# Optimization experiments

Measured on AMD Instinct MI355X. Metric: run time of the kernel, lower is better.

The kernel has to match this reference:

```python
import jax, jax.numpy as jnp
import numpy as np

# grid derived from output_shape=[1,10,200,176,128]: sparse_shape = (10+1, 200, 176)
D, H, W = 11, 200, 176
C_IN = 128
C_MID = 64
NUM_VOX = 16000
BN_EPS = 1e-5
DN = ('NCDHW', 'OIDHW', 'NCDHW')


def conv3d(x, w, stride, padding):
    return jax.lax.conv_general_dilated(x, w, window_strides=stride,
                                        padding=padding, dimension_numbers=DN)


def setup_inputs() -> dict:
    key = jax.random.key(0)
    ks = jax.random.split(key, 12)
    voxel_features = jax.random.normal(ks[0], (NUM_VOX, C_IN), dtype=jnp.float32)
    # unique active voxel coords (batch, z, y, x)
    lin = jax.random.choice(ks[1], D * H * W, (NUM_VOX,), replace=False)
    z = lin // (H * W)
    r = lin % (H * W)
    y = r // W
    x = r % W
    b = jnp.zeros((NUM_VOX,), dtype=jnp.int32)
    coors = jnp.stack([b, z.astype(jnp.int32), y.astype(jnp.int32), x.astype(jnp.int32)], axis=1)
    s = 0.05
    w1 = jax.random.normal(ks[2], (C_MID, C_IN, 3, 3, 3), jnp.float32) * s   # subm0
    w2 = jax.random.normal(ks[3], (C_MID, C_MID, 3, 1, 1), jnp.float32) * s  # strided
    w3 = jax.random.normal(ks[4], (C_MID, C_MID, 3, 3, 3), jnp.float32) * s  # subm1
    w4 = jax.random.normal(ks[5], (C_MID, C_MID, 3, 3, 3), jnp.float32) * s  # subm1
    w5 = jax.random.normal(ks[6], (C_MID, C_MID, 3, 1, 1), jnp.float32) * s  # strided
    bn_gamma = 1.0 + 0.1 * jax.random.normal(ks[7], (5, C_MID), jnp.float32)
    bn_beta = 0.1 * jax.random.normal(ks[8], (5, C_MID), jnp.float32)
    bn_mean = 0.1 * jax.random.normal(ks[9], (5, C_MID), jnp.float32)
    bn_var = 1.0 + 0.1 * jax.random.uniform(ks[10], (5, C_MID), jnp.float32)
    return {"voxel_features": voxel_features, "w1": w1, "w2": w2, "w3": w3,
            "w4": w4, "w5": w5, "bn_gamma": bn_gamma, "bn_beta": bn_beta,
            "bn_mean": bn_mean, "bn_var": bn_var, "coors": coors, "batch_size": 1}


def _bn_relu(x, i, mask, bn_gamma, bn_beta, bn_mean, bn_var):
    # inference-mode BatchNorm1d over active voxels (mask keeps inactive sites at 0)
    scale = (bn_gamma[i] / jnp.sqrt(bn_var[i] + BN_EPS))[None, :, None, None, None]
    shift = (bn_beta[i] - bn_mean[i] * bn_gamma[i] / jnp.sqrt(bn_var[i] + BN_EPS))[None, :, None, None, None]
    return jnp.maximum(x * scale + shift, 0.0) * mask


def reference(voxel_features, w1, w2, w3, w4, w5, bn_gamma, bn_beta, bn_mean, bn_var, coors, batch_size):
    N = int(batch_size)
    b, z, y, x = coors[:, 0], coors[:, 1], coors[:, 2], coors[:, 3]
    dense = jnp.zeros((N, C_IN, D, H, W), voxel_features.dtype).at[b, :, z, y, x].set(voxel_features)
    mask = jnp.zeros((N, 1, D, H, W), voxel_features.dtype).at[b, :, z, y, x].set(1.0)
    ones_k = jnp.ones((1, 1, 3, 1, 1), voxel_features.dtype)

    # SubMConv3d(128->64, k3, pad1): dense conv then restrict to active input sites
    h = conv3d(dense, w1, (1, 1, 1), [(1, 1), (1, 1), (1, 1)]) * mask
    h = _bn_relu(h, 0, mask, bn_gamma, bn_beta, bn_mean, bn_var)

    # SparseConv3d(64->64, k=(3,1,1), s=(2,1,1), pad0): new active set
    h = conv3d(h, w2, (2, 1, 1), 'VALID')
    mask = (conv3d(mask, ones_k, (2, 1, 1), 'VALID') > 0).astype(h.dtype)
    h = _bn_relu(h, 1, mask, bn_gamma, bn_beta, bn_mean, bn_var)

    # SubMConv3d(64->64) x2
    h = conv3d(h, w3, (1, 1, 1), [(1, 1), (1, 1), (1, 1)]) * mask
    h = _bn_relu(h, 2, mask, bn_gamma, bn_beta, bn_mean, bn_var)
    h = conv3d(h, w4, (1, 1, 1), [(1, 1), (1, 1), (1, 1)]) * mask
    h = _bn_relu(h, 3, mask, bn_gamma, bn_beta, bn_mean, bn_var)

    # SparseConv3d(64->64, (3,1,1), (2,1,1))
    h = conv3d(h, w5, (2, 1, 1), 'VALID')
    mask = (conv3d(mask, ones_k, (2, 1, 1), 'VALID') > 0).astype(h.dtype)
    h = _bn_relu(h, 4, mask, bn_gamma, bn_beta, bn_mean, bn_var)

    n, c, d, hh, ww = h.shape  # (1, 64, 2, 200, 176)
    return h.reshape(n, c * d, hh, ww)
```

## Files before the change

kernel.cpp:

```cpp
#include <hip/hip_runtime.h>

constexpr int D0  = 11;
constexpr int Hh  = 200;
constexpr int Ww  = 176;
constexpr int HWC = Hh * Ww;
constexpr int NV  = 16000;
constexpr int ND1 = 5;
constexpr int ND2 = 2;
constexpr int CAPN = 32000;
constexpr float EPS = 1e-5f;

constexpr int CAP1P  = 432000;
constexpr int CAP34P = 864000;
constexpr int CAP2P  = 32000;
constexpr int CAP5P  = 64000;

#define PC(i) ((i) << 5)

__device__ inline void wave_count(bool has, int* counter) {
    unsigned long long m = __ballot(has);
    int lane = threadIdx.x & 63;
    if (m && lane == __builtin_ctzll(m)) atomicAdd(counter, (int)__popcll(m));
}

__device__ inline int wave_append(bool has, int* counter) {
    unsigned long long m = __ballot(has);
    if (!m) return -1;
    int lane = threadIdx.x & 63;
    int leader = __builtin_ctzll(m);
    int base = 0;
    if (lane == leader) base = atomicAdd(counter, (int)__popcll(m));
    base = __shfl(base, leader);
    return has ? base + (int)__popcll(m & ((1ull << lane) - 1)) : -1;
}

__device__ inline int block_append(bool has, int* counter, int* lds) {
    int tid = threadIdx.x;
    int w = tid >> 6, lane = tid & 63;
    unsigned long long m = __ballot(has);
    if (lane == 0) lds[w] = (int)__popcll(m);
    __syncthreads();
    if (tid == 0) {
        int t0 = lds[0], t1 = lds[1], t2 = lds[2], t3 = lds[3];
        int base = atomicAdd(counter, t0 + t1 + t2 + t3);
        lds[4] = base;
        lds[5] = base + t0;
        lds[6] = base + t0 + t1;
        lds[7] = base + t0 + t1 + t2;
    }
    __syncthreads();
    int base = lds[4 + w];
    return has ? base + (int)__popcll(m & ((1ull << lane) - 1)) : -1;
}

__global__ __launch_bounds__(256) void setup1_k(const int* __restrict__ coors,
    int* __restrict__ grid0,
    const float* __restrict__ w1, const float* __restrict__ w2,
    const float* __restrict__ w3, const float* __restrict__ w4,
    const float* __restrict__ w5,
    float* __restrict__ w1t, float* __restrict__ w2t, float* __restrict__ w3t,
    float* __restrict__ w4t, float* __restrict__ w5t) {
    int idx = blockIdx.x * 256 + threadIdx.x;
    int role = blockIdx.y;
    if (role == 0) {
        if (idx < NV) {
            int4 c = reinterpret_cast<const int4*>(coors)[idx];
            grid0[c.y * HWC + c.z * Ww + c.w] = idx;
        }
        return;
    }
    const float* src; float* dst; int I, K;
    switch (role) {
        case 1:  src = w1; dst = w1t; I = 128; K = 27; break;
        case 2:  src = w2; dst = w2t; I = 64;  K = 3;  break;
        case 3:  src = w3; dst = w3t; I = 64;  K = 27; break;
        case 4:  src = w4; dst = w4t; I = 64;  K = 27; break;
        default: src = w5; dst = w5t; I = 64;  K = 3;  break;
    }
    int tot = 64 * I * K;
    if (idx >= tot) return;
    int o = idx / (I * K), r = idx % (I * K), ii = r / K, k = r % K;
    dst[(k * I + ii) * 64 + o] = src[idx];
}

__global__ __launch_bounds__(256) void setup2_k(const int* __restrict__ coors,
    const int* __restrict__ grid0, int* __restrict__ grid1,
    int* __restrict__ list1, int* __restrict__ list2, int* __restrict__ ctr) {
    __shared__ int lds[8];
    int idx = blockIdx.x * 256 + threadIdx.x;
    int role = blockIdx.y;
    if (role == 0) {
        bool occ = false; int p = idx;
        if (p < ND1 * HWC) {
            int d1 = p / HWC, yx = p - d1 * HWC;
            int b = (2 * d1) * HWC + yx;
            occ = (grid0[b] >= 0) || (grid0[b + HWC] >= 0) || (grid0[b + 2 * HWC] >= 0);
        }
        int s = block_append(occ, ctr + PC(0), lds);
        if (occ) { grid1[p] = s; list1[s] = p; }
    } else if (role == 1) {
        bool occ = false; int p = idx;
        if (p < ND2 * HWC) {
            int d2 = p / HWC, yx = p - d2 * HWC;
            #pragma unroll
            for (int dd = 0; dd < 7; ++dd) occ |= (grid0[(4 * d2 + dd) * HWC + yx] >= 0);
        }
        int s = block_append(occ, ctr + PC(1), lds);
        if (occ) list2[s] = p;
    } else {
        int k = idx / NV;
        bool has = false;
        if (idx < 27 * NV) {
            int i = idx - k * NV;
            int4 c = reinterpret_cast<const int4*>(coors)[i];
            int kd = k / 9, r = k % 9, kh = r / 3, kw = r % 3;
            int zz = c.y + kd - 1, yy = c.z + kh - 1, xx = c.w + kw - 1;
            if ((unsigned)zz < (unsigned)D0 && (unsigned)yy < (unsigned)Hh &&
                (unsigned)xx < (unsigned)Ww)
                has = grid0[zz * HWC + yy * Ww + xx] >= 0;
        }
        wave_count(has, ctr + PC(2 + k));
    }
}

__global__ __launch_bounds__(256) void setup3_k(const int* __restrict__ grid0,
    const int* __restrict__ grid1, const int* __restrict__ list1,
    const int* __restrict__ list2, int* __restrict__ ctr) {
    int idx = blockIdx.x * 256 + threadIdx.x;
    int role = blockIdx.y;
    int n1 = ctr[PC(0)], n2 = ctr[PC(1)];
    if (role == 0) {
        int k = idx / CAPN; bool has = false;
        if (idx < 3 * CAPN) {
            int s1 = idx - k * CAPN;
            if (s1 < n1) {
                int p = list1[s1]; int d1 = p / HWC, yx = p - d1 * HWC;
                has = grid0[(2 * d1 + k) * HWC + yx] >= 0;
            }
        }
        wave_count(has, ctr + PC(29 + k));
    } else if (role == 1) {
        int k = idx / CAPN; bool has = false;
        if (idx < 27 * CAPN) {
            int s1 = idx - k * CAPN;
            if (s1 < n1) {
                int p = list1[s1];
                int d1 = p / HWC, yx = p - d1 * HWC, y = yx / Ww, x = yx - y * Ww;
                int kd = k / 9, r = k % 9, kh = r / 3, kw = r % 3;
                int dd = d1 + kd - 1, yy = y + kh - 1, xx = x + kw - 1;
                if ((unsigned)dd < (unsigned)ND1 && (unsigned)yy < (unsigned)Hh &&
                    (unsigned)xx < (unsigned)Ww)
                    has = grid1[dd * HWC + yy * Ww + xx] >= 0;
            }
        }
        wave_count(has, ctr + PC(32 + k));
    } else {
        int k = idx / CAPN; bool has = false;
        if (idx < 3 * CAPN) {
            int s2 = idx - k * CAPN;
            if (s2 < n2) {
                int p = list2[s2]; int d2 = p / HWC, yx = p - d2 * HWC;
                has = grid1[(2 * d2 + k) * HWC + yx] >= 0;
            }
        }
        wave_count(has, ctr + PC(59 + k));
    }
}

__global__ __launch_bounds__(64) void setup4_k(const int* __restrict__ ctr,
    int* __restrict__ soff1, int* __restrict__ soff2,
    int* __restrict__ soff34, int* __restrict__ soff5) {
    int role = blockIdx.y, s = threadIdx.x;
    const int* cnt; int* soff; int NT, F;
    switch (role) {
        case 0:  cnt = ctr + PC(2);  soff = soff1;  NT = 27; F = 2; break;
        case 1:  cnt = ctr + PC(29); soff = soff2;  NT = 3;  F = 1; break;
        case 2:  cnt = ctr + PC(32); soff = soff34; NT = 27; F = 1; break;
        default: cnt = ctr + PC(59); soff = soff5;  NT = 3;  F = 1; break;
    }
    int tot = F * NT;
    if (s <= tot) {
        int sum = 0;
        for (int k = 0; k < NT; ++k) {
            int below = s - F * k;
            below = below < 0 ? 0 : (below > F ? F : below);
            sum += cnt[PC(k)] * below;
        }
        soff[s] = sum;
    }
}

__global__ __launch_bounds__(256) void setup5_k(const int* __restrict__ coors,
    const int* __restrict__ grid0, const int* __restrict__ grid1,
    const int* __restrict__ list1, const int* __restrict__ list2,
    int* __restrict__ ctr,
    const int* __restrict__ soff1, const int* __restrict__ soff2,
    const int* __restrict__ soff34, const int* __restrict__ soff5,
    int2* __restrict__ pairs1, int2* __restrict__ pairs2,
    int2* __restrict__ pairs34, int2* __restrict__ pairs5) {
    int idx = blockIdx.x * 256 + threadIdx.x;
    int role = blockIdx.y;
    int n1 = ctr[PC(0)], n2 = ctr[PC(1)];
    if (role == 0) {
        int k = idx / NV; bool has = false; int j = -1, i = 0;
        if (idx < 27 * NV) {
            i = idx - k * NV;
            int4 c = reinterpret_cast<const int4*>(coors)[i];
            int kd = k / 9, r = k % 9, kh = r / 3, kw = r % 3;
            int zz = c.y + kd - 1, yy = c.z + kh - 1, xx = c.w + kw - 1;
            if ((unsigned)zz < (unsigned)D0 && (unsigned)yy < (unsigned)Hh &&
                (unsigned)xx < (unsigned)Ww) {
                j = grid0[zz * HWC + yy * Ww + xx];
                has = j >= 0;
            }
        }
        int rel = wave_append(has, ctr + PC(62 + k));
        if (has) {
            int2 pr; pr.x = j; pr.y = i;
            pairs1[soff1[2 * k] + rel]     = pr;
            pairs1[soff1[2 * k + 1] + rel] = pr;
        }
    } else if (role == 1) {
        int k = idx / CAPN; bool has = false; int j = -1, s1 = 0;
        if (idx < 3 * CAPN) {
            s1 = idx - k * CAPN;
            if (s1 < n1) {
                int p = list1[s1]; int d1 = p / HWC, yx = p - d1 * HWC;
                j = grid0[(2 * d1 + k) * HWC + yx];
                has = j >= 0;
            }
        }
        int rel = wave_append(has, ctr + PC(89 + k));
        if (has) { int2 pr; pr.x = j; pr.y = s1; pairs2[soff2[k] + rel] = pr; }
    } else if (role == 2) {
        int k = idx / CAPN; bool has = false; int j = -1, s1 = 0;
        if (idx < 27 * CAPN) {
            s1 = idx - k * CAPN;
            if (s1 < n1) {
                int p = list1[s1];
                int d1 = p / HWC, yx = p - d1 * HWC, y = yx / Ww, x = yx - y * Ww;
                int kd = k / 9, r = k % 9, kh = r / 3, kw = r % 3;
                int dd = d1 + kd - 1, yy = y + kh - 1, xx = x + kw - 1;
                if ((unsigned)dd < (unsigned)ND1 && (unsigned)yy < (unsigned)Hh &&
                    (unsigned)xx < (unsigned)Ww) {
                    j = grid1[dd * HWC + yy * Ww + xx];
                    has = j >= 0;
                }
            }
        }
        int rel = wave_append(has, ctr + PC(92 + k));
        if (has) { int2 pr; pr.x = j; pr.y = s1; pairs34[soff34[k] + rel] = pr; }
    } else {
        int k = idx / CAPN; bool has = false; int j = -1, s2 = 0;
        if (idx < 3 * CAPN) {
            s2 = idx - k * CAPN;
            if (s2 < n2) {
                int p = list2[s2]; int d2 = p / HWC, yx = p - d2 * HWC;
                j = grid1[(2 * d2 + k) * HWC + yx];
                has = j >= 0;
            }
        }
        int rel = wave_append(has, ctr + PC(119 + k));
        if (has) { int2 pr; pr.x = j; pr.y = s2; pairs5[soff5[k] + rel] = pr; }
    }
}

template<int XS, bool HALF>
__global__ __launch_bounds__(256, 4) void pconv_k(
    const float* __restrict__ fin, const float* __restrict__ wt,
    const int2* __restrict__ pairs, const int* __restrict__ soff, int nslice,
    float* __restrict__ acc) {
    const int lane = threadIdx.x & 63;
    const int wid = __builtin_amdgcn_readfirstlane(
        (int)blockIdx.x * 4 + ((int)threadIdx.x >> 6));
    const int nw = (int)gridDim.x * 4;
    const int total = soff[nslice];
    int chunk = (total + nw - 1) / nw;
    int v = wid * chunk;
    int v1 = v + chunk; if (v1 > total) v1 = total;
    if (v >= v1) return;

    int lo = 0, hi = nslice - 1;
    while (lo < hi) { int mid = (lo + hi + 1) >> 1; if (soff[mid] <= v) lo = mid; else hi = mid - 1; }
    int s = lo, send = soff[s + 1];

    float w[64];
    int xofs = 0;
    bool need = true;
    while (v < v1) {
        while (v >= send) { ++s; send = soff[s + 1]; need = true; }
        if (need) {
            const float* wp = wt + (size_t)s * 4096 + lane;
            #pragma unroll
            for (int c = 0; c < 64; ++c) w[c] = wp[(size_t)c * 64];
            if (HALF) xofs = (s & 1) * 64;
            need = false;
        }
        int e = v1 < send ? v1 : send;
        for (; v + 1 < e; v += 2) {
            int2 prA = pairs[v];
            int2 prB = pairs[v + 1];
            int ja = __builtin_amdgcn_readfirstlane(prA.x);
            int ya = __builtin_amdgcn_readfirstlane(prA.y);
            int jb = __builtin_amdgcn_readfirstlane(prB.x);
            int yb = __builtin_amdgcn_readfirstlane(prB.y);
            const float* xa = fin + (size_t)ja * XS + xofs;
            const float* xb = fin + (size_t)jb * XS + xofs;
            float a0=0.f,a1=0.f,a2=0.f,a3=0.f,b0=0.f,b1=0.f,b2=0.f,b3=0.f;
            #pragma unroll
            for (int c = 0; c < 64; c += 4) {
                a0 = fmaf(xa[c],     w[c],     a0);
                a1 = fmaf(xa[c + 1], w[c + 1], a1);
                a2 = fmaf(xa[c + 2], w[c + 2], a2);
                a3 = fmaf(xa[c + 3], w[c + 3], a3);
                b0 = fmaf(xb[c],     w[c],     b0);
                b1 = fmaf(xb[c + 1], w[c + 1], b1);
                b2 = fmaf(xb[c + 2], w[c + 2], b2);
                b3 = fmaf(xb[c + 3], w[c + 3], b3);
            }
            unsafeAtomicAdd(acc + ((size_t)ya << 6) + lane, (a0 + a1) + (a2 + a3));
            unsafeAtomicAdd(acc + ((size_t)yb << 6) + lane, (b0 + b1) + (b2 + b3));
        }
        if (v < e) {
            int2 pr = pairs[v]; ++v;
            int jp = __builtin_amdgcn_readfirstlane(pr.x);
            int yp = __builtin_amdgcn_readfirstlane(pr.y);
            const float* xp = fin + (size_t)jp * XS + xofs;
            float a0=0.f,a1=0.f,a2=0.f,a3=0.f;
            #pragma unroll
            for (int c = 0; c < 64; c += 4) {
                a0 = fmaf(xp[c],     w[c],     a0);
                a1 = fmaf(xp[c + 1], w[c + 1], a1);
                a2 = fmaf(xp[c + 2], w[c + 2], a2);
                a3 = fmaf(xp[c + 3], w[c + 3], a3);
            }
            unsafeAtomicAdd(acc + ((size_t)yp << 6) + lane, (a0 + a1) + (a2 + a3));
        }
    }
}

template<bool ZERO, bool FIXEDN>
__global__ __launch_bounds__(256) void bn_k(float* __restrict__ acc,
    float* __restrict__ f, const int* __restrict__ ctr,
    const float* __restrict__ bg, const float* __restrict__ bb,
    const float* __restrict__ bm, const float* __restrict__ bv) {
    int idx = blockIdx.x * 256 + threadIdx.x;
    int site = idx >> 6, o = idx & 63;
    int n = FIXEDN ? NV : ctr[PC(0)];
    if (site < n) {
        float sc = bg[o] / sqrtf(bv[o] + EPS);
        float sh = bb[o] - bm[o] * sc;
        f[idx] = fmaxf(fmaf(acc[idx], sc, sh), 0.f);
    }
    if (ZERO) acc[idx] = 0.f;
}

__global__ __launch_bounds__(256) void bn5_k(const float* __restrict__ acc5,
    const int* __restrict__ list2, const int* __restrict__ ctr,
    const float* __restrict__ bg, const float* __restrict__ bb,
    const float* __restrict__ bm, const float* __restrict__ bv,
    float* __restrict__ out) {
    __shared__ float tile[64 * 65];
    __shared__ int pp[64];
    int n2 = ctr[PC(1)];
    int sb = blockIdx.x * 64;
    int tid = threadIdx.x;
    if (tid < 64) pp[tid] = (sb + tid < n2) ? list2[sb + tid] : -1;
    int o = tid & 63;
    float sc = bg[o] / sqrtf(bv[o] + EPS);
    float sh = bb[o] - bm[o] * sc;
    __syncthreads();
    #pragma unroll
    for (int it = 0; it < 16; ++it) {
        int sl = it * 4 + (tid >> 6);
        int s2 = sb + sl;
        if (s2 < n2)
            tile[sl * 65 + o] = fmaxf(fmaf(acc5[(size_t)s2 * 64 + o], sc, sh), 0.f);
    }
    __syncthreads();
    #pragma unroll
    for (int it = 0; it < 16; ++it) {
        int og = it * 4 + (tid >> 6);
        int sl = tid & 63;
        int p = pp[sl];
        if (p >= 0) {
            int d2 = p / HWC, yx = p - d2 * HWC;
            out[(size_t)(og * ND2 + d2) * HWC + yx] = tile[sl * 65 + og];
        }
    }
}

extern "C" void kernel_launch(void* const* d_in, const int* in_sizes, int n_in,
                              void* d_out, int out_size, void* d_ws, size_t ws_size,
                              hipStream_t stream) {
    const float* vf = (const float*)d_in[0];
    const float* w1 = (const float*)d_in[1];
    const float* w2 = (const float*)d_in[2];
    const float* w3 = (const float*)d_in[3];
    const float* w4 = (const float*)d_in[4];
    const float* w5 = (const float*)d_in[5];
    const float* bg = (const float*)d_in[6];
    const float* bb = (const float*)d_in[7];
    const float* bm = (const float*)d_in[8];
    const float* bv = (const float*)d_in[9];
    const int* coors = (const int*)d_in[10];
    float* out = (float*)d_out;

    char* ws = (char*)d_ws;
    size_t off = 0;
    auto take = [&](size_t n) -> void* {
        void* pp = ws + off;
        off += (n + 255) & ~(size_t)255;
        return pp;
    };
    int*   ctr  = (int*)take(16384);
    float* acc1 = (float*)take((size_t)NV * 64 * 4);
    float* accX = (float*)take((size_t)CAPN * 64 * 4);
    float* acc5 = (float*)take((size_t)CAPN * 64 * 4);
    size_t zero_len = (char*)acc5 + (size_t)CAPN * 64 * 4 - (char*)ctr;
    int*   grid0 = (int*)take((size_t)D0 * HWC * 4);
    int*   grid1 = (int*)take((size_t)ND1 * HWC * 4);
    size_t ff_len = (char*)grid1 + (size_t)ND1 * HWC * 4 - (char*)grid0;
    int*   list1 = (int*)take(CAPN * 4);
    int*   list2 = (int*)take(CAPN * 4);
    int*   soff1 = (int*)take(256);
    int*   soff2 = (int*)take(256);
    int*   soff34 = (int*)take(256);
    int*   soff5 = (int*)take(256);
    float* w1t = (float*)take((size_t)27 * 128 * 64 * 4);
    float* w2t = (float*)take((size_t)3 * 64 * 64 * 4);
    float* w3t = (float*)take((size_t)27 * 64 * 64 * 4);
    float* w4t = (float*)take((size_t)27 * 64 * 64 * 4);
    float* w5t = (float*)take((size_t)3 * 64 * 64 * 4);
    float* fA  = (float*)take((size_t)NV * 64 * 4);
    float* fB  = (float*)take((size_t)CAPN * 64 * 4);
    int2*  pairs1  = (int2*)take((size_t)2 * CAP1P * 8);
    int2*  pairs2  = (int2*)take((size_t)CAP2P * 8);
    int2*  pairs34 = (int2*)take((size_t)CAP34P * 8);
    int2*  pairs5  = (int2*)take((size_t)CAP5P * 8);

    hipMemsetAsync(ctr, 0x00, zero_len, stream);
    hipMemsetAsync(grid0, 0xFF, ff_len, stream);
    hipMemsetAsync(out, 0x00, (size_t)out_size * 4, stream);

    setup1_k<<<dim3(864, 6), 256, 0, stream>>>(coors, grid0, w1, w2, w3, w4, w5,
                                               w1t, w2t, w3t, w4t, w5t);
    setup2_k<<<dim3(1688, 3), 256, 0, stream>>>(coors, grid0, grid1, list1, list2, ctr);
    setup3_k<<<dim3(3375, 3), 256, 0, stream>>>(grid0, grid1, list1, list2, ctr);
    setup4_k<<<dim3(1, 4), 64, 0, stream>>>(ctr, soff1, soff2, soff34, soff5);
    setup5_k<<<dim3(3375, 4), 256, 0, stream>>>(coors, grid0, grid1, list1, list2, ctr,
                                                soff1, soff2, soff34, soff5,
                                                pairs1, pairs2, pairs34, pairs5);

    pconv_k<128, true><<<1024, 256, 0, stream>>>(vf, w1t, pairs1, soff1, 54, acc1);
    bn_k<false, true><<<(NV * 64) / 256, 256, 0, stream>>>(acc1, fA, ctr,
        bg, bb, bm, bv);
    pconv_k<64, false><<<1024, 256, 0, stream>>>(fA, w2t, pairs2, soff2, 3, accX);
    bn_k<true, false><<<(CAPN * 64) / 256, 256, 0, stream>>>(accX, fB, ctr,
        bg + 64, bb + 64, bm + 64, bv + 64);
    pconv_k<64, false><<<1024, 256, 0, stream>>>(fB, w3t, pairs34, soff34, 27, accX);
    bn_k<true, false><<<(CAPN * 64) / 256, 256, 0, stream>>>(accX, fB, ctr,
        bg + 128, bb + 128, bm + 128, bv + 128);
    pconv_k<64, false><<<1024, 256, 0, stream>>>(fB, w4t, pairs34, soff34, 27, accX);
    bn_k<false, false><<<(CAPN * 64) / 256, 256, 0, stream>>>(accX, fB, ctr,
        bg + 192, bb + 192, bm + 192, bv + 192);
    pconv_k<64, false><<<1024, 256, 0, stream>>>(fB, w5t, pairs5, soff5, 3, acc5);
    bn5_k<<<CAPN / 64, 256, 0, stream>>>(acc5, list2, ctr,
        bg + 256, bb + 256, bm + 256, bv + 256, out);
}
```

Measured before the change: 279.9 us.

## Build rulebook pairs in one pass with fixed-stride slices instead of count+scan+fill

After: 248.9 us. -11.1%, faster.

```diff
diff --git a/kernel.cpp b/kernel.cpp
--- a/kernel.cpp
+++ b/kernel.cpp
@@ -10,18 +10,7 @@
 constexpr int CAPN = 32000;
 constexpr float EPS = 1e-5f;
 
-constexpr int CAP1P  = 432000;
-constexpr int CAP34P = 864000;
-constexpr int CAP2P  = 32000;
-constexpr int CAP5P  = 64000;
-
 #define PC(i) ((i) << 5)
-
-__device__ inline void wave_count(bool has, int* counter) {
-    unsigned long long m = __ballot(has);
-    int lane = threadIdx.x & 63;
-    if (m && lane == __builtin_ctzll(m)) atomicAdd(counter, (int)__popcll(m));
-}
 
 __device__ inline int wave_append(bool has, int* counter) {
     unsigned long long m = __ballot(has);
@@ -85,12 +74,13 @@
 
 __global__ __launch_bounds__(256) void setup2_k(const int* __restrict__ coors,
     const int* __restrict__ grid0, int* __restrict__ grid1,
-    int* __restrict__ list1, int* __restrict__ list2, int* __restrict__ ctr) {
+    int* __restrict__ list1, int* __restrict__ list2, int* __restrict__ ctr,
+    int2* __restrict__ pairs1) {
     __shared__ int lds[8];
-    int idx = blockIdx.x * 256 + threadIdx.x;
-    int role = blockIdx.y;
-    if (role == 0) {
-        bool occ = false; int p = idx;
+    int bid = blockIdx.x, tid = threadIdx.x;
+    if (bid < 688) {
+        int p = bid * 256 + tid;
+        bool occ = false;
         if (p < ND1 * HWC) {
             int d1 = p / HWC, yx = p - d1 * HWC;
             int b = (2 * d1) * HWC + yx;
@@ -98,8 +88,9 @@
         }
         int s = block_append(occ, ctr + PC(0), lds);
         if (occ) { grid1[p] = s; list1[s] = p; }
-    } else if (role == 1) {
-        bool occ = false; int p = idx;
+    } else if (bid < 963) {
+        int p = (bid - 688) * 256 + tid;
+        bool occ = false;
         if (p < ND2 * HWC) {
             int d2 = p / HWC, yx = p - d2 * HWC;
             #pragma unroll
@@ -108,103 +99,11 @@
         int s = block_append(occ, ctr + PC(1), lds);
         if (occ) list2[s] = p;
     } else {
+        int idx = (bid - 963) * 256 + tid;
         int k = idx / NV;
-        bool has = false;
+        bool has = false; int j = -1;
+        int i = idx - k * NV;
         if (idx < 27 * NV) {
-            int i = idx - k * NV;
-            int4 c = reinterpret_cast<const int4*>(coors)[i];
-            int kd = k / 9, r = k % 9, kh = r / 3, kw = r % 3;
-            int zz = c.y + kd - 1, yy = c.z + kh - 1, xx = c.w + kw - 1;
-            if ((unsigned)zz < (unsigned)D0 && (unsigned)yy < (unsigned)Hh &&
-                (unsigned)xx < (unsigned)Ww)
-                has = grid0[zz * HWC + yy * Ww + xx] >= 0;
-        }
-        wave_count(has, ctr + PC(2 + k));
-    }
-}
-
-__global__ __launch_bounds__(256) void setup3_k(const int* __restrict__ grid0,
-    const int* __restrict__ grid1, const int* __restrict__ list1,
-    const int* __restrict__ list2, int* __restrict__ ctr) {
-    int idx = blockIdx.x * 256 + threadIdx.x;
-    int role = blockIdx.y;
-    int n1 = ctr[PC(0)], n2 = ctr[PC(1)];
-    if (role == 0) {
-        int k = idx / CAPN; bool has = false;
-        if (idx < 3 * CAPN) {
-            int s1 = idx - k * CAPN;
-            if (s1 < n1) {
-                int p = list1[s1]; int d1 = p / HWC, yx = p - d1 * HWC;
-                has = grid0[(2 * d1 + k) * HWC + yx] >= 0;
-            }
-        }
-        wave_count(has, ctr + PC(29 + k));
-    } else if (role == 1) {
-        int k = idx / CAPN; bool has = false;
-        if (idx < 27 * CAPN) {
-            int s1 = idx - k * CAPN;
-            if (s1 < n1) {
-                int p = list1[s1];
-                int d1 = p / HWC, yx = p - d1 * HWC, y = yx / Ww, x = yx - y * Ww;
-                int kd = k / 9, r = k % 9, kh = r / 3, kw = r % 3;
-                int dd = d1 + kd - 1, yy = y + kh - 1, xx = x + kw - 1;
-                if ((unsigned)dd < (unsigned)ND1 && (unsigned)yy < (unsigned)Hh &&
-                    (unsigned)xx < (unsigned)Ww)
-                    has = grid1[dd * HWC + yy * Ww + xx] >= 0;
-            }
-        }
-        wave_count(has, ctr + PC(32 + k));
-    } else {
-        int k = idx / CAPN; bool has = false;
-        if (idx < 3 * CAPN) {
-            int s2 = idx - k * CAPN;
-            if (s2 < n2) {
-                int p = list2[s2]; int d2 = p / HWC, yx = p - d2 * HWC;
-                has = grid1[(2 * d2 + k) * HWC + yx] >= 0;
-            }
-        }
-        wave_count(has, ctr + PC(59 + k));
-    }
-}
-
-__global__ __launch_bounds__(64) void setup4_k(const int* __restrict__ ctr,
-    int* __restrict__ soff1, int* __restrict__ soff2,
-    int* __restrict__ soff34, int* __restrict__ soff5) {
-    int role = blockIdx.y, s = threadIdx.x;
-    const int* cnt; int* soff; int NT, F;
-    switch (role) {
-        case 0:  cnt = ctr + PC(2);  soff = soff1;  NT = 27; F = 2; break;
-        case 1:  cnt = ctr + PC(29); soff = soff2;  NT = 3;  F = 1; break;
-        case 2:  cnt = ctr + PC(32); soff = soff34; NT = 27; F = 1; break;
-        default: cnt = ctr + PC(59); soff = soff5;  NT = 3;  F = 1; break;
-    }
-    int tot = F * NT;
-    if (s <= tot) {
-        int sum = 0;
-        for (int k = 0; k < NT; ++k) {
-            int below = s - F * k;
-            below = below < 0 ? 0 : (below > F ? F : below);
-            sum += cnt[PC(k)] * below;
-        }
-        soff[s] = sum;
-    }
-}
-
-__global__ __launch_bounds__(256) void setup5_k(const int* __restrict__ coors,
-    const int* __restrict__ grid0, const int* __restrict__ grid1,
-    const int* __restrict__ list1, const int* __restrict__ list2,
-    int* __restrict__ ctr,
-    const int* __restrict__ soff1, const int* __restrict__ soff2,
-    const int* __restrict__ soff34, const int* __restrict__ soff5,
-    int2* __restrict__ pairs1, int2* __restrict__ pairs2,
-    int2* __restrict__ pairs34, int2* __restrict__ pairs5) {
-    int idx = blockIdx.x * 256 + threadIdx.x;
-    int role = blockIdx.y;
-    int n1 = ctr[PC(0)], n2 = ctr[PC(1)];
-    if (role == 0) {
-        int k = idx / NV; bool has = false; int j = -1, i = 0;
-        if (idx < 27 * NV) {
-            i = idx - k * NV;
             int4 c = reinterpret_cast<const int4*>(coors)[i];
             int kd = k / 9, r = k % 9, kh = r / 3, kw = r % 3;
             int zz = c.y + kd - 1, yy = c.z + kh - 1, xx = c.w + kw - 1;
@@ -214,92 +113,105 @@
                 has = j >= 0;
             }
         }
-        int rel = wave_append(has, ctr + PC(62 + k));
-        if (has) {
-            int2 pr; pr.x = j; pr.y = i;
-            pairs1[soff1[2 * k] + rel]     = pr;
-            pairs1[soff1[2 * k + 1] + rel] = pr;
-        }
-    } else if (role == 1) {
-        int k = idx / CAPN; bool has = false; int j = -1, s1 = 0;
-        if (idx < 3 * CAPN) {
-            s1 = idx - k * CAPN;
-            if (s1 < n1) {
-                int p = list1[s1]; int d1 = p / HWC, yx = p - d1 * HWC;
-                j = grid0[(2 * d1 + k) * HWC + yx];
+        int rel = wave_append(has, ctr + PC(2 + k));
+        if (has) { int2 pr; pr.x = j; pr.y = i; pairs1[k * NV + rel] = pr; }
+    }
+}
+
+__global__ __launch_bounds__(256) void setup3_k(const int* __restrict__ grid0,
+    const int* __restrict__ grid1, const int* __restrict__ list1,
+    const int* __restrict__ list2, int* __restrict__ ctr,
+    int2* __restrict__ pairs2, int2* __restrict__ pairs34,
+    int2* __restrict__ pairs5) {
+    int bid = blockIdx.x, tid = threadIdx.x;
+    int n1 = ctr[PC(0)], n2 = ctr[PC(1)];
+    if (bid < 375) {
+        int idx = bid * 256 + tid;
+        int k = idx / CAPN;
+        int s1 = idx - k * CAPN;
+        bool has = false; int j = -1;
+        if (s1 < n1) {
+            int p = list1[s1]; int d1 = p / HWC, yx = p - d1 * HWC;
+            j = grid0[(2 * d1 + k) * HWC + yx];
+            has = j >= 0;
+        }
+        int rel = wave_append(has, ctr + PC(29 + k));
+        if (has) { int2 pr; pr.x = j; pr.y = s1; pairs2[k * CAPN + rel] = pr; }
+    } else if (bid < 3750) {
+        int idx = (bid - 375) * 256 + tid;
+        int k = idx / CAPN;
+        int s1 = idx - k * CAPN;
+        bool has = false; int j = -1;
+        if (s1 < n1) {
+            int p = list1[s1];
+            int d1 = p / HWC, yx = p - d1 * HWC, y = yx / Ww, x = yx - y * Ww;
+            int kd = k / 9, r = k % 9, kh = r / 3, kw = r % 3;
+            int dd = d1 + kd - 1, yy = y + kh - 1, xx = x + kw - 1;
+            if ((unsigned)dd < (unsigned)ND1 && (unsigned)yy < (unsigned)Hh &&
+                (unsigned)xx < (unsigned)Ww) {
+                j = grid1[dd * HWC + yy * Ww + xx];
                 has = j >= 0;
             }
         }
-        int rel = wave_append(has, ctr + PC(89 + k));
-        if (has) { int2 pr; pr.x = j; pr.y = s1; pairs2[soff2[k] + rel] = pr; }
-    } else if (role == 2) {
-        int k = idx / CAPN; bool has = false; int j = -1, s1 = 0;
-        if (idx < 27 * CAPN) {
-            s1 = idx - k * CAPN;
-            if (s1 < n1) {
-                int p = list1[s1];
-                int d1 = p / HWC, yx = p - d1 * HWC, y = yx / Ww, x = yx - y * Ww;
-                int kd = k / 9, r = k % 9, kh = r / 3, kw = r % 3;
-                int dd = d1 + kd - 1, yy = y + kh - 1, xx = x + kw - 1;
-                if ((unsigned)dd < (unsigned)ND1 && (unsigned)yy < (unsigned)Hh &&
-                    (unsigned)xx < (unsigned)Ww) {
-                    j = grid1[dd * HWC + yy * Ww + xx];
-                    has = j >= 0;
-                }
-            }
-        }
-        int rel = wave_append(has, ctr + PC(92 + k));
-        if (has) { int2 pr; pr.x = j; pr.y = s1; pairs34[soff34[k] + rel] = pr; }
+        int rel = wave_append(has, ctr + PC(32 + k));
+        if (has) { int2 pr; pr.x = j; pr.y = s1; pairs34[k * CAPN + rel] = pr; }
     } else {
-        int k = idx / CAPN; bool has = false; int j = -1, s2 = 0;
-        if (idx < 3 * CAPN) {
-            s2 = idx - k * CAPN;
-            if (s2 < n2) {
-                int p = list2[s2]; int d2 = p / HWC, yx = p - d2 * HWC;
-                j = grid1[(2 * d2 + k) * HWC + yx];
-                has = j >= 0;
-            }
-        }
-        int rel = wave_append(has, ctr + PC(119 + k));
-        if (has) { int2 pr; pr.x = j; pr.y = s2; pairs5[soff5[k] + rel] = pr; }
-    }
-}
-
-template<int XS, bool HALF>
+        int idx = (bid - 3750) * 256 + tid;
+        int k = idx / CAPN;
+        int s2 = idx - k * CAPN;
+        bool has = false; int j = -1;
+        if (s2 < n2) {
+            int p = list2[s2]; int d2 = p / HWC, yx = p - d2 * HWC;
+            j = grid1[(2 * d2 + k) * HWC + yx];
+            has = j >= 0;
+        }
+        int rel = wave_append(has, ctr + PC(59 + k));
+        if (has) { int2 pr; pr.x = j; pr.y = s2; pairs5[k * CAPN + rel] = pr; }
+    }
+}
+
+template<int XS, bool HALF, int NT, int STRIDE>
 __global__ __launch_bounds__(256, 4) void pconv_k(
     const float* __restrict__ fin, const float* __restrict__ wt,
-    const int2* __restrict__ pairs, const int* __restrict__ soff, int nslice,
+    const int2* __restrict__ pairs, const int* __restrict__ cnt,
     float* __restrict__ acc) {
     const int lane = threadIdx.x & 63;
     const int wid = __builtin_amdgcn_readfirstlane(
         (int)blockIdx.x * 4 + ((int)threadIdx.x >> 6));
     const int nw = (int)gridDim.x * 4;
-    const int total = soff[nslice];
+
+    int sum = 0;
+    #pragma unroll
+    for (int k = 0; k < NT; ++k) sum += cnt[k << 5];
+    const int total = HALF ? 2 * sum : sum;
+
     int chunk = (total + nw - 1) / nw;
     int v = wid * chunk;
     int v1 = v + chunk; if (v1 > total) v1 = total;
     if (v >= v1) return;
 
-    int lo = 0, hi = nslice - 1;
-    while (lo < hi) { int mid = (lo + hi + 1) >> 1; if (soff[mid] <= v) lo = mid; else hi = mid - 1; }
-    int s = lo, send = soff[s + 1];
+    int s = 0, soff_s = 0;
+    int send = cnt[0];
+    while (v >= send) { soff_s = send; ++s; send += cnt[(HALF ? (s >> 1) : s) << 5]; }
 
     float w[64];
     int xofs = 0;
+    const int2* pb = nullptr;
     bool need = true;
     while (v < v1) {
-        while (v >= send) { ++s; send = soff[s + 1]; need = true; }
+        while (v >= send) { soff_s = send; ++s; send += cnt[(HALF ? (s >> 1) : s) << 5]; need = true; }
         if (need) {
             const float* wp = wt + (size_t)s * 4096 + lane;
             #pragma unroll
             for (int c = 0; c < 64; ++c) w[c] = wp[(size_t)c * 64];
             if (HALF) xofs = (s & 1) * 64;
+            pb = pairs + (size_t)(HALF ? (s >> 1) : s) * STRIDE - soff_s;
             need = false;
         }
         int e = v1 < send ? v1 : send;
         for (; v + 1 < e; v += 2) {
-            int2 prA = pairs[v];
-            int2 prB = pairs[v + 1];
+            int2 prA = pb[v];
+            int2 prB = pb[v + 1];
             int ja = __builtin_amdgcn_readfirstlane(prA.x);
             int ya = __builtin_amdgcn_readfirstlane(prA.y);
             int jb = __builtin_amdgcn_readfirstlane(prB.x);
@@ -322,7 +234,7 @@
             unsafeAtomicAdd(acc + ((size_t)yb << 6) + lane, (b0 + b1) + (b2 + b3));
         }
         if (v < e) {
-            int2 pr = pairs[v]; ++v;
+            int2 pr = pb[v]; ++v;
             int jp = __builtin_amdgcn_readfirstlane(pr.x);
             int yp = __builtin_amdgcn_readfirstlane(pr.y);
             const float* xp = fin + (size_t)jp * XS + xofs;
@@ -351,8 +263,8 @@
         float sc = bg[o] / sqrtf(bv[o] + EPS);
         float sh = bb[o] - bm[o] * sc;
         f[idx] = fmaxf(fmaf(acc[idx], sc, sh), 0.f);
-    }
-    if (ZERO) acc[idx] = 0.f;
+        if (ZERO) acc[idx] = 0.f;
+    }
 }
 
 __global__ __launch_bounds__(256) void bn5_k(const float* __restrict__ acc5,
@@ -423,10 +335,6 @@
     size_t ff_len = (char*)grid1 + (size_t)ND1 * HWC * 4 - (char*)grid0;
     int*   list1 = (int*)take(CAPN * 4);
     int*   list2 = (int*)take(CAPN * 4);
-    int*   soff1 = (int*)take(256);
-    int*   soff2 = (int*)take(256);
-    int*   soff34 = (int*)take(256);
-    int*   soff5 = (int*)take(256);
     float* w1t = (float*)take((size_t)27 * 128 * 64 * 4);
     float* w2t = (float*)take((size_t)3 * 64 * 64 * 4);
     float* w3t = (float*)take((size_t)27 * 64 * 64 * 4);
@@ -434,10 +342,10 @@
     float* w5t = (float*)take((size_t)3 * 64 * 64 * 4);
     float* fA  = (float*)take((size_t)NV * 64 * 4);
     float* fB  = (float*)take((size_t)CAPN * 64 * 4);
-    int2*  pairs1  = (int2*)take((size_t)2 * CAP1P * 8);
-    int2*  pairs2  = (int2*)take((size_t)CAP2P * 8);
-    int2*  pairs34 = (int2*)take((size_t)CAP34P * 8);
-    int2*  pairs5  = (int2*)take((size_t)CAP5P * 8);
+    int2*  pairs1  = (int2*)take((size_t)27 * NV * 8);
+    int2*  pairs2  = (int2*)take((size_t)3 * CAPN * 8);
+    int2*  pairs34 = (int2*)take((size_t)27 * CAPN * 8);
+    int2*  pairs5  = (int2*)take((size_t)3 * CAPN * 8);
 
     hipMemsetAsync(ctr, 0x00, zero_len, stream);
     hipMemsetAsync(grid0, 0xFF, ff_len, stream);
@@ -445,26 +353,28 @@
 
     setup1_k<<<dim3(864, 6), 256, 0, stream>>>(coors, grid0, w1, w2, w3, w4, w5,
                                                w1t, w2t, w3t, w4t, w5t);
-    setup2_k<<<dim3(1688, 3), 256, 0, stream>>>(coors, grid0, grid1, list1, list2, ctr);
-    setup3_k<<<dim3(3375, 3), 256, 0, stream>>>(grid0, grid1, list1, list2, ctr);
-    setup4_k<<<dim3(1, 4), 64, 0, stream>>>(ctr, soff1, soff2, soff34, soff5);
-    setup5_k<<<dim3(3375, 4), 256, 0, stream>>>(coors, grid0, grid1, list1, list2, ctr,
-                                                soff1, soff2, soff34, soff5,
-                                                pairs1, pairs2, pairs34, pairs5);
-
-    pconv_k<128, true><<<1024, 256, 0, stream>>>(vf, w1t, pairs1, soff1, 54, acc1);
+    setup2_k<<<2651, 256, 0, stream>>>(coors, grid0, grid1, list1, list2, ctr, pairs1);
+    setup3_k<<<4125, 256, 0, stream>>>(grid0, grid1, list1, list2, ctr,
+                                       pairs2, pairs34, pairs5);
+
+    pconv_k<128, true, 27, NV><<<1024, 256, 0, stream>>>(vf, w1t, pairs1,
+                                                         ctr + PC(2), acc1);
     bn_k<false, true><<<(NV * 64) / 256, 256, 0, stream>>>(acc1, fA, ctr,
         bg, bb, bm, bv);
-    pconv_k<64, false><<<1024, 256, 0, stream>>>(fA, w2t, pairs2, soff2, 3, accX);
+    pconv_k<64, false, 3, CAPN><<<1024, 256, 0, stream>>>(fA, w2t, pairs2,
+                                                          ctr + PC(29), accX);
     bn_k<true, false><<<(CAPN * 64) / 256, 256, 0, stream>>>(accX, fB, ctr,
         bg + 64, bb + 64, bm + 64, bv + 64);
-    pconv_k<64, false><<<1024, 256, 0, stream>>>(fB, w3t, pairs34, soff34, 27, accX);
+    pconv_k<64, false, 27, CAPN><<<1024, 256, 0, stream>>>(fB, w3t, pairs34,
+                                                           ctr + PC(32), accX);
     bn_k<true, false><<<(CAPN * 64) / 256, 256, 0, stream>>>(accX, fB, ctr,
         bg + 128, bb + 128, bm + 128, bv + 128);
-    pconv_k<64, false><<<1024, 256, 0, stream>>>(fB, w4t, pairs34, soff34, 27, accX);
+    pconv_k<64, false, 27, CAPN><<<1024, 256, 0, stream>>>(fB, w4t, pairs34,
+                                                           ctr + PC(32), accX);
     bn_k<false, false><<<(CAPN * 64) / 256, 256, 0, stream>>>(accX, fB, ctr,
         bg + 192, bb + 192, bm + 192, bv + 192);
-    pconv_k<64, false><<<1024, 256, 0, stream>>>(fB, w5t, pairs5, soff5, 3, acc5);
+    pconv_k<64, false, 3, CAPN><<<1024, 256, 0, stream>>>(fB, w5t, pairs5,
+                                                          ctr + PC(59), acc5);
     bn5_k<<<CAPN / 64, 256, 0, stream>>>(acc5, list2, ctr,
         bg + 256, bb + 256, bm + 256, bv + 256, out);
 }
```
